# Kernel tuning notes

Measured on AMD Instinct MI355X. Metric: run time of the kernel, lower is better.

Reference implementation:

```python
import jax, jax.numpy as jnp
import numpy as np

B, H, CO, NV, NQ = 16, 1024, 512, 2048, 2048

def setup_inputs() -> dict:
    key = jax.random.key(0)
    ks = jax.random.split(key, 7)
    return {
        "V": jax.random.normal(ks[0], (B, H, NV), dtype=jnp.float32),
        "Q": jax.random.normal(ks[1], (B, NQ, H), dtype=jnp.float32),
        "W_b": jax.random.normal(ks[2], (H, H), dtype=jnp.float32),
        "W_v": jax.random.normal(ks[3], (CO, H), dtype=jnp.float32),
        "W_q": jax.random.normal(ks[4], (CO, H), dtype=jnp.float32),
        "w_hv": jax.random.normal(ks[5], (CO, 1), dtype=jnp.float32),
        "w_hq": jax.random.normal(ks[6], (CO, 1), dtype=jnp.float32),
    }

def reference(V, Q, W_b, W_v, W_q, w_hv, w_hq):
    # C = Q @ (W_b @ V): [B, Nq, Nv]
    WbV = jnp.einsum('hk,bkv->bhv', W_b, V)
    C = jnp.einsum('bqh,bhv->bqv', Q, WbV)
    WvV = jnp.einsum('ch,bhv->bcv', W_v, V)          # [B, CO, Nv]
    WqQt = jnp.einsum('ch,bqh->bcq', W_q, Q)         # [B, CO, Nq]
    H_v = jnp.tanh(WvV + jnp.einsum('bcq,bqv->bcv', WqQt, C))   # [B, CO, Nv]
    H_q = jnp.tanh(WqQt + jnp.einsum('bcv,bqv->bcq', WvV, C))   # [B, CO, Nq]
    a_v = jax.nn.softmax(jnp.einsum('c,bcv->bv', w_hv[:, 0], H_v), axis=-1)[:, None, :]  # [B,1,Nv]
    a_q = jax.nn.softmax(jnp.einsum('c,bcq->bq', w_hq[:, 0], H_q), axis=-1)[:, None, :]  # [B,1,Nq]
    v = jnp.einsum('bv,bhv->bh', a_v[:, 0], V)   # [B, H]
    q = jnp.einsum('bq,bqh->bh', a_q[:, 0], Q)   # [B, H]
    return (a_v, a_q, v, q)
```

## Files before the change

kernel.cpp:

```cpp
#include <hip/hip_runtime.h>
#include <math.h>

#define Bn  16
#define Hd  1024
#define COn 512
#define NVn 2048
#define NQn 2048

#define BM 128
#define BN 128
#define BK 16
#define LDT 132

typedef unsigned short u16;
typedef __attribute__((ext_vector_type(8))) short short8;
typedef __attribute__((ext_vector_type(4))) float floatx4;

__device__ __forceinline__ float fast_tanh(float x) {
    float ax = fabsf(x);
    float e  = __expf(2.0f * ax);
    float t  = 1.0f - 2.0f / (e + 1.0f);
    return copysignf(t, x);
}

__device__ __forceinline__ u16 f32_to_bf16(float x) {
    unsigned u = __float_as_uint(x);
    unsigned r = (u + 0x7fffu + ((u >> 16) & 1u)) >> 16;
    return (u16)r;
}
__device__ __forceinline__ float bf16_to_f32(u16 h) {
    return __uint_as_float(((unsigned)h) << 16);
}

__device__ __forceinline__ void gload16(const u16* g, u16* l) {
    __builtin_amdgcn_global_load_lds(
        (__attribute__((address_space(1))) void*)(g),
        (__attribute__((address_space(3))) void*)(l), 16, 0, 0);
}

template <bool LOGITS>
__global__ __launch_bounds__(512, 2) void mm8p(
    const u16* __restrict__ Ahp, const u16* __restrict__ Alp, long batchA, int ldA,
    const u16* __restrict__ Bhp, const u16* __restrict__ Blp, long batchB, int ldB,
    int N, int K, int gx, int gy,
    const float* __restrict__ bias,
    u16* __restrict__ Ch, u16* __restrict__ Cl, long batchC,
    const float* __restrict__ w, float* __restrict__ logits)
{
    __shared__ u16 lds[2][4][256 * 32];

    const int tid = threadIdx.x;
    const int nwg = (int)gridDim.x;
    int bid = (int)blockIdx.x;
    {
        int q = nwg >> 3, r = nwg & 7, xcd = bid & 7, idx = bid >> 3;
        bid = (xcd < r ? xcd * (q + 1) : r * (q + 1) + (xcd - r) * q) + idx;
    }
    const int bpz = gx * gy;
    const int b    = bid / bpz;
    const int brem = bid - b * bpz;
    const int m0 = (brem / gx) * 256;
    const int n0 = (brem % gx) * 256;

    const u16* Ahb = Ahp + (long)b * batchA;
    const u16* Alb = Alp + (long)b * batchA;
    const u16* Bhb = Bhp + (long)b * batchB;
    const u16* Blb = Blp + (long)b * batchB;

    const int wave = tid >> 6, lane = tid & 63;
    const int quad = lane >> 4, l16 = lane & 15;
    const int wm = (wave >> 2) * 128;
    const int wn = (wave & 3) * 64;
    const int aoff = quad * 8;

    const int smat  = wave >> 1;
    const int srow0 = (wave & 1) * 128;
    const int srl   = lane >> 2;
    const int ssl   = (lane & 3) * 8;
    const u16* srcp = smat == 0 ? Ahb : smat == 1 ? Alb : smat == 2 ? Bhb : Blb;
    const long sld  = (smat < 2) ? ldA : ldB;
    const int rowbase = (smat < 2) ? m0 : n0;
    const u16* sp = srcp + (long)(rowbase + srow0 + srl) * sld + ssl;

    floatx4 acc[8][4] = {};

#pragma unroll
    for (int j = 0; j < 8; ++j)
        gload16(sp + (long)j * 16 * sld, &lds[0][smat][(srow0 + j * 16) * 32]);
    asm volatile("s_waitcnt vmcnt(0)" ::: "memory");
    __builtin_amdgcn_s_barrier();

    const int NT = K >> 5;
    for (int t = 0; t < NT; ++t) {
        const int  cur = t & 1;
        const bool pf  = (t + 1 < NT);
        const long k0n = (long)(t + 1) * 32;
        const u16* Ah_ = &lds[cur][0][0];
        const u16* Al_ = &lds[cur][1][0];
        const u16* Bh_ = &lds[cur][2][0];
        const u16* Bl_ = &lds[cur][3][0];
        short8 bh[4], bl[4];
#pragma unroll
        for (int p = 0; p < 4; ++p) {
            if (p == 0) {
#pragma unroll
                for (int nt = 0; nt < 4; ++nt) {
                    const int br = (wn + nt * 16 + l16) * 32 + aoff;
                    bh[nt] = *(const short8*)&Bh_[br];
                    bl[nt] = *(const short8*)&Bl_[br];
                }
            }
            const int ar0 = (wm + (2 * p) * 16 + l16) * 32 + aoff;
            const int ar1 = ar0 + 16 * 32;
            const short8 a0h = *(const short8*)&Ah_[ar0];
            const short8 a0l = *(const short8*)&Al_[ar0];
            const short8 a1h = *(const short8*)&Ah_[ar1];
            const short8 a1l = *(const short8*)&Al_[ar1];
            if (pf && p < 2) {
                const int tb = cur ^ 1;
#pragma unroll
                for (int j = p * 4; j < p * 4 + 4; ++j)
                    gload16(sp + (long)j * 16 * sld + k0n,
                            &lds[tb][smat][(srow0 + j * 16) * 32]);
            }
            __builtin_amdgcn_s_barrier();
            __builtin_amdgcn_s_setprio(1);
#pragma unroll
            for (int nt = 0; nt < 4; ++nt) {
                floatx4 c0 = acc[2 * p][nt];
                c0 = __builtin_amdgcn_mfma_f32_16x16x32_bf16(a0h, bh[nt], c0, 0, 0, 0);
                c0 = __builtin_amdgcn_mfma_f32_16x16x32_bf16(a0h, bl[nt], c0, 0, 0, 0);
                c0 = __builtin_amdgcn_mfma_f32_16x16x32_bf16(a0l, bh[nt], c0, 0, 0, 0);
                acc[2 * p][nt] = c0;
                floatx4 c1 = acc[2 * p + 1][nt];
                c1 = __builtin_amdgcn_mfma_f32_16x16x32_bf16(a1h, bh[nt], c1, 0, 0, 0);
                c1 = __builtin_amdgcn_mfma_f32_16x16x32_bf16(a1h, bl[nt], c1, 0, 0, 0);
                c1 = __builtin_amdgcn_mfma_f32_16x16x32_bf16(a1l, bh[nt], c1, 0, 0, 0);
                acc[2 * p + 1][nt] = c1;
            }
            __builtin_amdgcn_s_setprio(0);
            if (p == 3 && pf) asm volatile("s_waitcnt vmcnt(0)" ::: "memory");
            __builtin_amdgcn_s_barrier();
        }
    }

    if constexpr (!LOGITS) {
        u16* Chb = Ch + (long)b * batchC;
        u16* Clb = Cl + (long)b * batchC;
#pragma unroll
        for (int mt = 0; mt < 8; ++mt)
#pragma unroll
            for (int nt = 0; nt < 4; ++nt)
#pragma unroll
                for (int r = 0; r < 4; ++r) {
                    const int row = m0 + wm + mt * 16 + quad * 4 + r;
                    const int col = n0 + wn + nt * 16 + l16;
                    float x = acc[mt][nt][r];
                    if (bias) x += bias[(long)row * N + col];
                    const u16 h = f32_to_bf16(x);
                    Chb[(long)row * N + col] = h;
                    Clb[(long)row * N + col] = f32_to_bf16(x - bf16_to_f32(h));
                }
    } else {
        float cs[4] = {};
#pragma unroll
        for (int nt = 0; nt < 4; ++nt)
#pragma unroll
            for (int mt = 0; mt < 8; ++mt)
#pragma unroll
                for (int r = 0; r < 4; ++r) {
                    const int row = m0 + wm + mt * 16 + quad * 4 + r;
                    cs[nt] = fmaf(w[row], fast_tanh(acc[mt][nt][r]), cs[nt]);
                }
        float* red = (float*)&lds[0][0][0];
        const int r8 = (wave >> 2) * 4 + quad;
#pragma unroll
        for (int nt = 0; nt < 4; ++nt)
            red[r8 * 256 + wn + nt * 16 + l16] = cs[nt];
        __syncthreads();
        if (tid < 256) {
            float s = 0.f;
#pragma unroll
            for (int r = 0; r < 8; ++r) s += red[r * 256 + tid];
            atomicAdd(logits + (long)b * N + n0 + tid, s);
        }
    }
}

template <bool LOGITS>
__global__ __launch_bounds__(256) void mm3(
    const u16* __restrict__ Ahp, const u16* __restrict__ Alp, long batchA, int ldA,
    const u16* __restrict__ Bhp, const u16* __restrict__ Blp, long batchB, int ldB,
    int N, int K,
    const float* __restrict__ bias,
    u16* __restrict__ Ch, u16* __restrict__ Cl, long batchC,
    const float* __restrict__ w, float* __restrict__ logits)
{
    __shared__ u16 Ah[128 * 32], Al[128 * 32], Bh[128 * 32], Bl[128 * 32];
    const int tid = threadIdx.x;
    const int b   = blockIdx.z;
    const int m0  = blockIdx.y * 128;
    const int n0  = blockIdx.x * 128;
    const u16* Ahb = Ahp + (long)b * batchA;
    const u16* Alb = Alp + (long)b * batchA;
    const u16* Bhb = Bhp + (long)b * batchB;
    const u16* Blb = Blp + (long)b * batchB;
    const int wave = tid >> 6, lane = tid & 63, quad = lane >> 4, l16 = lane & 15;
    const int wm = (wave >> 1) * 64, wn = (wave & 1) * 64;
    floatx4 acc[4][4] = {};

    for (int k0 = 0; k0 < K; k0 += 32) {
#pragma unroll
        for (int i = 0; i < 2; ++i) {
            int c = i * 256 + tid;
            int row = c >> 2, ko = (c & 3) * 8;
            long ga = (long)(m0 + row) * ldA + k0 + ko;
            long gb = (long)(n0 + row) * ldB + k0 + ko;
            *(short8*)&Ah[row * 32 + ko] = *(const short8*)&Ahb[ga];
            *(short8*)&Al[row * 32 + ko] = *(const short8*)&Alb[ga];
            *(short8*)&Bh[row * 32 + ko] = *(const short8*)&Bhb[gb];
            *(short8*)&Bl[row * 32 + ko] = *(const short8*)&Blb[gb];
        }
        __syncthreads();
        short8 ah[4], al[4], bh[4], bl[4];
#pragma unroll
        for (int t4 = 0; t4 < 4; ++t4) {
            int am = wm + t4 * 16 + l16;
            ah[t4] = *(const short8*)&Ah[am * 32 + quad * 8];
            al[t4] = *(const short8*)&Al[am * 32 + quad * 8];
            int bn = wn + t4 * 16 + l16;
            bh[t4] = *(const short8*)&Bh[bn * 32 + quad * 8];
            bl[t4] = *(const short8*)&Bl[bn * 32 + quad * 8];
        }
#pragma unroll
        for (int mt = 0; mt < 4; ++mt)
#pragma unroll
            for (int nt = 0; nt < 4; ++nt) {
                floatx4 a0 = acc[mt][nt];
                a0 = __builtin_amdgcn_mfma_f32_16x16x32_bf16(ah[mt], bh[nt], a0, 0, 0, 0);
                a0 = __builtin_amdgcn_mfma_f32_16x16x32_bf16(ah[mt], bl[nt], a0, 0, 0, 0);
                a0 = __builtin_amdgcn_mfma_f32_16x16x32_bf16(al[mt], bh[nt], a0, 0, 0, 0);
                acc[mt][nt] = a0;
            }
        __syncthreads();
    }

    if constexpr (!LOGITS) {
        u16* Chb = Ch + (long)b * batchC;
        u16* Clb = Cl + (long)b * batchC;
#pragma unroll
        for (int mt = 0; mt < 4; ++mt)
#pragma unroll
            for (int nt = 0; nt < 4; ++nt)
#pragma unroll
                for (int r = 0; r < 4; ++r) {
                    int row = m0 + wm + mt * 16 + quad * 4 + r;
                    int col = n0 + wn + nt * 16 + l16;
                    float x = acc[mt][nt][r];
                    if (bias) x += bias[(long)row * N + col];
                    u16 h = f32_to_bf16(x);
                    u16 l = f32_to_bf16(x - bf16_to_f32(h));
                    Chb[(long)row * N + col] = h;
                    Clb[(long)row * N + col] = l;
                }
    } else {
        float cs[4] = {};
#pragma unroll
        for (int nt = 0; nt < 4; ++nt)
#pragma unroll
            for (int mt = 0; mt < 4; ++mt)
#pragma unroll
                for (int r = 0; r < 4; ++r) {
                    int row = m0 + wm + mt * 16 + quad * 4 + r;
                    cs[nt] = fmaf(w[row], fast_tanh(acc[mt][nt][r]), cs[nt]);
                }
        float* red = (float*)Ah;
        const int r8 = (wave >> 1) * 4 + quad;
#pragma unroll
        for (int nt = 0; nt < 4; ++nt)
            red[r8 * 128 + wn + nt * 16 + l16] = cs[nt];
        __syncthreads();
        if (tid < 128) {
            float s = 0.f;
#pragma unroll
            for (int r = 0; r < 8; ++r) s += red[r * 128 + tid];
            atomicAdd(logits + (long)b * N + n0 + tid, s);
        }
    }
}

__global__ __launch_bounds__(256) void split_kernel(
    const float* __restrict__ X, u16* __restrict__ Xh, u16* __restrict__ Xl)
{
    long i0 = ((long)blockIdx.x * 256 + threadIdx.x) * 4;
    float4 v = *(const float4*)(X + i0);
    float xs[4] = {v.x, v.y, v.z, v.w};
    u16 h[4], l[4];
#pragma unroll
    for (int i = 0; i < 4; ++i) {
        h[i] = f32_to_bf16(xs[i]);
        l[i] = f32_to_bf16(xs[i] - bf16_to_f32(h[i]));
    }
    *(ushort4*)(Xh + i0) = *(ushort4*)h;
    *(ushort4*)(Xl + i0) = *(ushort4*)l;
}

__global__ __launch_bounds__(256) void tsplit_kernel(
    const float* __restrict__ src, u16* __restrict__ dh, u16* __restrict__ dl,
    int R, int C)
{
    __shared__ float tile[64][65];
    const int b = blockIdx.z;
    const int r0 = blockIdx.x * 64, c0 = blockIdx.y * 64;
    const float* S = src + (long)b * R * C;
    const int t = threadIdx.x;
    const int lr = t >> 2, lc0 = (t & 3) * 16;
#pragma unroll
    for (int i = 0; i < 4; ++i)
        *(float4*)&tile[lr][lc0 + i * 4] =
            *(const float4*)(S + (long)(r0 + lr) * C + c0 + lc0 + i * 4);
    __syncthreads();
    u16 hbuf[16], lbuf[16];
#pragma unroll
    for (int i = 0; i < 16; ++i) {
        float x = tile[lc0 + i][lr];
        u16 hi = f32_to_bf16(x);
        hbuf[i] = hi;
        lbuf[i] = f32_to_bf16(x - bf16_to_f32(hi));
    }
    long o = (long)b * R * C + (long)(c0 + lr) * R + r0 + lc0;
    *(short8*)(dh + o)     = *(short8*)&hbuf[0];
    *(short8*)(dh + o + 8) = *(short8*)&hbuf[8];
    *(short8*)(dl + o)     = *(short8*)&lbuf[0];
    *(short8*)(dl + o + 8) = *(short8*)&lbuf[8];
}

template <bool LOGITS>
__global__ __launch_bounds__(256) void gemm_core(
    const float* __restrict__ A, const float* __restrict__ Bm, float* __restrict__ C,
    const float* __restrict__ bias,
    int M, int N, int K,
    int sAm, int sAk, long batchA,
    int sBk, int sBn, long batchB,
    long batchC,
    const float* __restrict__ w, float* __restrict__ logits)
{
    __shared__ float As[BK][LDT];
    __shared__ float Bs[BK][LDT];
    const int tid = threadIdx.x;
    const int b   = blockIdx.z;
    const int m0  = blockIdx.y * BM;
    const int n0  = blockIdx.x * BN;
    const float* Ab = A  + (long)b * batchA;
    const float* Bb = Bm + (long)b * batchB;
    const int tm = tid >> 4, tn = tid & 15;
    float acc[8][8] = {};

    for (int k0 = 0; k0 < K; k0 += BK) {
        if (sAk == 1) {
#pragma unroll
            for (int i = 0; i < 2; ++i) {
                int idx = tid + i * 256;
                int m = idx >> 2, kg = (idx & 3) * 4;
                float4 v = *(const float4*)(Ab + (long)(m0 + m) * sAm + k0 + kg);
                As[kg+0][m] = v.x; As[kg+1][m] = v.y; As[kg+2][m] = v.z; As[kg+3][m] = v.w;
            }
        } else {
#pragma unroll
            for (int i = 0; i < 2; ++i) {
                int idx = tid + i * 256;
                int k = idx >> 5, mg = (idx & 31) * 4;
                float4 v = *(const float4*)(Ab + (long)(k0 + k) * sAk + m0 + mg);
                *(float4*)&As[k][mg] = v;
            }
        }
        if (sBn == 1) {
#pragma unroll
            for (int i = 0; i < 2; ++i) {
                int idx = tid + i * 256;
                int k = idx >> 5, ng = (idx & 31) * 4;
                float4 v = *(const float4*)(Bb + (long)(k0 + k) * sBk + n0 + ng);
                *(float4*)&Bs[k][ng] = v;
            }
        } else {
#pragma unroll
            for (int i = 0; i < 2; ++i) {
                int idx = tid + i * 256;
                int n = idx >> 2, kg = (idx & 3) * 4;
                float4 v = *(const float4*)(Bb + (long)(n0 + n) * sBn + k0 + kg);
                Bs[kg+0][n] = v.x; Bs[kg+1][n] = v.y; Bs[kg+2][n] = v.z; Bs[kg+3][n] = v.w;
            }
        }
        __syncthreads();
#pragma unroll
        for (int kk = 0; kk < BK; ++kk) {
            float a[8], bv[8];
            *(float4*)&a[0]  = *(const float4*)&As[kk][tm * 4];
            *(float4*)&a[4]  = *(const float4*)&As[kk][64 + tm * 4];
            *(float4*)&bv[0] = *(const float4*)&Bs[kk][tn * 4];
            *(float4*)&bv[4] = *(const float4*)&Bs[kk][64 + tn * 4];
#pragma unroll
            for (int i = 0; i < 8; ++i)
#pragma unroll
                for (int j = 0; j < 8; ++j)
                    acc[i][j] = fmaf(a[i], bv[j], acc[i][j]);
        }
        __syncthreads();
    }

    if constexpr (!LOGITS) {
        float* Cb = C + (long)b * batchC;
#pragma unroll
        for (int i = 0; i < 8; ++i) {
            int row = m0 + (i >> 2) * 64 + tm * 4 + (i & 3);
            float* crow = Cb + (long)row * N + n0;
            float4 o0 = {acc[i][0], acc[i][1], acc[i][2], acc[i][3]};
            float4 o1 = {acc[i][4], acc[i][5], acc[i][6], acc[i][7]};
            if (bias) {
                const float* brow = bias + (long)row * N + n0;
                float4 b0 = *(const float4*)(brow + tn * 4);
                float4 b1 = *(const float4*)(brow + 64 + tn * 4);
                o0.x += b0.x; o0.y += b0.y; o0.z += b0.z; o0.w += b0.w;
                o1.x += b1.x; o1.y += b1.y; o1.z += b1.z; o1.w += b1.w;
            }
            *(float4*)(crow + tn * 4) = o0;
            *(float4*)(crow + 64 + tn * 4) = o1;
        }
    } else {
        float wv[8];
#pragma unroll
        for (int i = 0; i < 8; ++i) wv[i] = w[m0 + (i >> 2) * 64 + tm * 4 + (i & 3)];
        float cs[8];
#pragma unroll
        for (int j = 0; j < 8; ++j) {
            float s = 0.f;
#pragma unroll
            for (int i = 0; i < 8; ++i) s = fmaf(wv[i], fast_tanh(acc[i][j]), s);
            cs[j] = s;
        }
        __syncthreads();
        *(float4*)&As[tm][tn * 4]      = *(float4*)&cs[0];
        *(float4*)&As[tm][64 + tn * 4] = *(float4*)&cs[4];
        __syncthreads();
        if (tid < 128) {
            float s = 0.f;
#pragma unroll
            for (int r = 0; r < 16; ++r) s += As[r][tid];
            atomicAdd(logits + (long)b * N + n0 + tid, s);
        }
    }
}

__global__ __launch_bounds__(256) void softmax_kernel(
    const float* __restrict__ lv, const float* __restrict__ lq, float* __restrict__ out)
{
    const int b = blockIdx.x;
    const int which = blockIdx.y;
    const float* x = (which == 0 ? lv : lq) + (long)b * 2048;
    float* o = out + (long)which * (Bn * 2048) + (long)b * 2048;
    const int tid = threadIdx.x;
    __shared__ float sm[4], ss[4];

    float m = -3.4e38f;
    for (int i = tid; i < 2048; i += 256) m = fmaxf(m, x[i]);
    for (int off = 32; off > 0; off >>= 1) m = fmaxf(m, __shfl_down(m, off));
    if ((tid & 63) == 0) sm[tid >> 6] = m;
    __syncthreads();
    m = fmaxf(fmaxf(sm[0], sm[1]), fmaxf(sm[2], sm[3]));

    float s = 0.f;
    for (int i = tid; i < 2048; i += 256) s += expf(x[i] - m);
    for (int off = 32; off > 0; off >>= 1) s += __shfl_down(s, off);
    if ((tid & 63) == 0) ss[tid >> 6] = s;
    __syncthreads();
    s = ss[0] + ss[1] + ss[2] + ss[3];
    float inv = 1.0f / s;
    for (int i = tid; i < 2048; i += 256) o[i] = expf(x[i] - m) * inv;
}

__global__ __launch_bounds__(256) void vout_kernel(
    const float* __restrict__ V, const float* __restrict__ av, float* __restrict__ vout)
{
    const int wave = threadIdx.x >> 6, lane = threadIdx.x & 63;
    const long idx = (long)blockIdx.x * 4 + wave;
    const int b = (int)(idx >> 10);
    const int h = (int)(idx & 1023);
    const float* vp = V + ((long)b * Hd + h) * NVn;
    const float* ap = av + (long)b * NVn;
    float s = 0.f;
    for (int i = lane; i < NVn; i += 64) s = fmaf(ap[i], vp[i], s);
    for (int off = 32; off > 0; off >>= 1) s += __shfl_down(s, off);
    if (lane == 0) vout[idx] = s;
}

__global__ __launch_bounds__(256) void qout_kernel(
    const float* __restrict__ Q, const float* __restrict__ aq, float* __restrict__ qout)
{
    const int h  = blockIdx.x * 256 + threadIdx.x;
    const int b  = blockIdx.z;
    const int q0 = blockIdx.y * 256;
    const float* qp = Q + (long)b * NQn * Hd;
    const float* ap = aq + (long)b * NQn + q0;
    float s = 0.f;
    for (int q = 0; q < 256; ++q) s = fmaf(ap[q], qp[(long)(q0 + q) * Hd + h], s);
    atomicAdd(qout + (long)b * Hd + h, s);
}

extern "C" void kernel_launch(void* const* d_in, const int* in_sizes, int n_in,
                              void* d_out, int out_size, void* d_ws, size_t ws_size,
                              hipStream_t stream) {
    const float* V    = (const float*)d_in[0];
    const float* Q    = (const float*)d_in[1];
    const float* W_b  = (const float*)d_in[2];
    const float* W_v  = (const float*)d_in[3];
    const float* W_q  = (const float*)d_in[4];
    const float* w_hv = (const float*)d_in[5];
    const float* w_hq = (const float*)d_in[6];
    float* out = (float*)d_out;
    dim3 blk(256);

    const long BIG  = (long)Bn * Hd * NVn;
    const long GEL  = (long)Bn * Hd * Hd;
    const long TEL  = (long)Bn * COn * Hd;
    const long WQE  = (long)COn * Hd;
    const long WBE  = (long)Hd * Hd;

    u16* ws16 = (u16*)d_ws;
    u16* R1h  = ws16;            u16* R1l  = R1h + BIG;
    u16* Gh   = R1l + BIG;       u16* Gl   = Gh + GEL;
    u16* Th   = Gl + GEL;        u16* Tl   = Th + TEL;
    u16* Uh   = Gh;              u16* Ul   = Gh + TEL;
    u16* Wqh  = Tl + TEL;        u16* Wql  = Wqh + WQE;
    u16* Wvh  = Wql + WQE;       u16* Wvl  = Wvh + WQE;
    u16* Wbh  = Wvl + WQE;       u16* Wbl  = Wbh + WBE;
    u16* WbTh = Wbl + WBE;       u16* WbTl = WbTh + WBE;
    float* lv = (float*)(WbTl + WBE);
    float* lq = lv + Bn * NVn;
    const size_t need = (size_t)((u16*)(lq + Bn * NQn) - ws16) * 2;

    float* vout_p = out + 2 * Bn * NVn;
    float* qout_p = vout_p + Bn * Hd;

    if (ws_size >= need) {
        hipMemsetAsync(lv, 0, (size_t)(Bn * NVn + Bn * NQn) * sizeof(float), stream);
        hipMemsetAsync(qout_p, 0, (size_t)Bn * Hd * sizeof(float), stream);

        split_kernel<<<dim3((unsigned)(WQE / 1024)), blk, 0, stream>>>(W_q, Wqh, Wql);
        split_kernel<<<dim3((unsigned)(WQE / 1024)), blk, 0, stream>>>(W_v, Wvh, Wvl);
        split_kernel<<<dim3((unsigned)(WBE / 1024)), blk, 0, stream>>>(W_b, Wbh, Wbl);
        tsplit_kernel<<<dim3(Hd / 64, Hd / 64, 1), blk, 0, stream>>>(W_b, WbTh, WbTl, Hd, Hd);

        tsplit_kernel<<<dim3(NQn / 64, Hd / 64, Bn), blk, 0, stream>>>(Q, R1h, R1l, NQn, Hd);
        mm8p<false><<<dim3((Hd / 256) * (Hd / 256) * Bn), dim3(512), 0, stream>>>(
            R1h, R1l, (long)Hd * NQn, NQn,  R1h, R1l, (long)Hd * NQn, NQn,
            Hd, NQn, Hd / 256, Hd / 256,
            nullptr, Gh, Gl, (long)Hd * Hd, nullptr, nullptr);
        mm3<false><<<dim3(Hd / 128, COn / 128, Bn), blk, 0, stream>>>(
            Wqh, Wql, 0L, Hd,  Gh, Gl, (long)Hd * Hd, Hd,
            Hd, Hd, nullptr, Th, Tl, (long)COn * Hd, nullptr, nullptr);
        mm3<false><<<dim3(Hd / 128, COn / 128, Bn), blk, 0, stream>>>(
            Th, Tl, (long)COn * Hd, Hd,  WbTh, WbTl, 0L, Hd,
            Hd, Hd, W_v, Uh, Ul, (long)COn * Hd, nullptr, nullptr);
        tsplit_kernel<<<dim3(Hd / 64, NVn / 64, Bn), blk, 0, stream>>>(V, R1h, R1l, Hd, NVn);
        mm8p<true><<<dim3((NVn / 256) * (COn / 256) * Bn), dim3(512), 0, stream>>>(
            Uh, Ul, (long)COn * Hd, Hd,  R1h, R1l, (long)NVn * Hd, Hd,
            NVn, Hd, NVn / 256, COn / 256,
            nullptr, nullptr, nullptr, 0L, w_hv, lv);

        split_kernel<<<dim3((unsigned)(BIG / 1024)), blk, 0, stream>>>(V, R1h, R1l);
        mm8p<false><<<dim3((Hd / 256) * (Hd / 256) * Bn), dim3(512), 0, stream>>>(
            R1h, R1l, (long)Hd * NVn, NVn,  R1h, R1l, (long)Hd * NVn, NVn,
            Hd, NVn, Hd / 256, Hd / 256,
            nullptr, Gh, Gl, (long)Hd * Hd, nullptr, nullptr);
        mm3<false><<<dim3(Hd / 128, COn / 128, Bn), blk, 0, stream>>>(
            Wvh, Wvl, 0L, Hd,  Gh, Gl, (long)Hd * Hd, Hd,
            Hd, Hd, nullptr, Th, Tl, (long)COn * Hd, nullptr, nullptr);
        mm3<false><<<dim3(Hd / 128, COn / 128, Bn), blk, 0, stream>>>(
            Th, Tl, (long)COn * Hd, Hd,  Wbh, Wbl, 0L, Hd,
            Hd, Hd, W_q, Uh, Ul, (long)COn * Hd, nullptr, nullptr);
        split_kernel<<<dim3((unsigned)(BIG / 1024)), blk, 0, stream>>>(Q, R1h, R1l);
        mm8p<true><<<dim3((NQn / 256) * (COn / 256) * Bn), dim3(512), 0, stream>>>(
            Uh, Ul, (long)COn * Hd, Hd,  R1h, R1l, (long)NQn * Hd, Hd,
            NQn, Hd, NQn / 256, COn / 256,
            nullptr, nullptr, nullptr, 0L, w_hq, lq);

        softmax_kernel<<<dim3(Bn, 2), blk, 0, stream>>>(lv, lq, out);
        vout_kernel<<<dim3(Bn * Hd / 4), blk, 0, stream>>>(V, out, vout_p);
        qout_kernel<<<dim3(Hd / 256, NQn / 256, Bn), blk, 0, stream>>>(Q, out + Bn * NVn, qout_p);
        return;
    }

    float* ws = (float*)d_ws;
    float* g  = ws;
    float* t  = g + GEL;
    float* u  = t + TEL;
    float* flv = u + TEL;
    float* flq = flv + Bn * NVn;

    hipMemsetAsync(flv, 0, (size_t)(Bn * NVn + Bn * NQn) * sizeof(float), stream);
    hipMemsetAsync(qout_p, 0, (size_t)Bn * Hd * sizeof(float), stream);

    gemm_core<false><<<dim3(Hd/BN, Hd/BM, Bn), blk, 0, stream>>>(Q, Q, g, nullptr,
        Hd, Hd, NQn, 1, Hd, (long)NQn*Hd, Hd, 1, (long)NQn*Hd, (long)Hd*Hd, nullptr, nullptr);
    gemm_core<false><<<dim3(Hd/BN, COn/BM, Bn), blk, 0, stream>>>(W_q, g, t, nullptr,
        COn, Hd, Hd, Hd, 1, 0L, Hd, 1, (long)Hd*Hd, (long)COn*Hd, nullptr, nullptr);
    gemm_core<false><<<dim3(Hd/BN, COn/BM, Bn), blk, 0, stream>>>(t, W_b, u, W_v,
        COn, Hd, Hd, Hd, 1, (long)COn*Hd, Hd, 1, 0L, (long)COn*Hd, nullptr, nullptr);
    gemm_core<true><<<dim3(NVn/BN, COn/BM, Bn), blk, 0, stream>>>(
        u, V, nullptr, nullptr, COn, NVn, Hd,
        Hd, 1, (long)COn*Hd, NVn, 1, (long)Hd*NVn, 0L, w_hv, flv);
    gemm_core<false><<<dim3(Hd/BN, Hd/BM, Bn), blk, 0, stream>>>(V, V, g, nullptr,
        Hd, Hd, NVn, NVn, 1, (long)Hd*NVn, 1, NVn, (long)Hd*NVn, (long)Hd*Hd, nullptr, nullptr);
    gemm_core<false><<<dim3(Hd/BN, COn/BM, Bn), blk, 0, stream>>>(W_v, g, t, nullptr,
        COn, Hd, Hd, Hd, 1, 0L, Hd, 1, (long)Hd*Hd, (long)COn*Hd, nullptr, nullptr);
    gemm_core<false><<<dim3(Hd/BN, COn/BM, Bn), blk, 0, stream>>>(t, W_b, u, W_q,
        COn, Hd, Hd, Hd, 1, (long)COn*Hd, 1, Hd, 0L, (long)COn*Hd, nullptr, nullptr);
    gemm_core<true><<<dim3(NQn/BN, COn/BM, Bn), blk, 0, stream>>>(
        u, Q, nullptr, nullptr, COn, NQn, Hd,
        Hd, 1, (long)COn*Hd, 1, Hd, (long)NQn*Hd, 0L, w_hq, flq);

    softmax_kernel<<<dim3(Bn, 2), blk, 0, stream>>>(flv, flq, out);
    vout_kernel<<<dim3(Bn * Hd / 4), blk, 0, stream>>>(V, out, vout_p);
    qout_kernel<<<dim3(Hd / 256, NQn / 256, Bn), blk, 0, stream>>>(Q, out + Bn * NVn, qout_p);
}
```

Measured before the change: 1.275 ms.

## XOR-swizzle LDS tiles and issue full prefetch once per K-step

Applies an XOR swizzle to the K-chunk position of both the staged LDS tiles and the fragment reads, in both GEMM kernels, so that lanes reading 16-byte fragments hit different LDS banks. The swizzle is applied on the global-read side for the direct-to-LDS loads. The main kernel also issues all eight prefetch loads at once after loading B fragments, and drops the per-phase barriers, leaving a single wait and barrier per K-step. The aim is fewer bank conflicts and less synchronisation, at the risk of less even interleaving of memory traffic with MFMA work.

```diff
diff --git a/kernel.cpp b/kernel.cpp
--- a/kernel.cpp
+++ b/kernel.cpp
@@ -69,18 +69,18 @@
 
     const int wave = tid >> 6, lane = tid & 63;
     const int quad = lane >> 4, l16 = lane & 15;
+    const int xsl = (quad ^ ((l16 >> 1) & 3)) * 8;
     const int wm = (wave >> 2) * 128;
     const int wn = (wave & 3) * 64;
-    const int aoff = quad * 8;
 
     const int smat  = wave >> 1;
     const int srow0 = (wave & 1) * 128;
     const int srl   = lane >> 2;
-    const int ssl   = (lane & 3) * 8;
+    const int kx    = ((lane & 3) ^ ((lane >> 3) & 3)) * 8;
     const u16* srcp = smat == 0 ? Ahb : smat == 1 ? Alb : smat == 2 ? Bhb : Blb;
     const long sld  = (smat < 2) ? ldA : ldB;
     const int rowbase = (smat < 2) ? m0 : n0;
-    const u16* sp = srcp + (long)(rowbase + srow0 + srl) * sld + ssl;
+    const u16* sp = srcp + (long)(rowbase + srow0 + srl) * sld + kx;
 
     floatx4 acc[8][4] = {};
 
@@ -99,31 +99,28 @@
         const u16* Al_ = &lds[cur][1][0];
         const u16* Bh_ = &lds[cur][2][0];
         const u16* Bl_ = &lds[cur][3][0];
+
         short8 bh[4], bl[4];
 #pragma unroll
+        for (int nt = 0; nt < 4; ++nt) {
+            const int bs = (wn + nt * 16 + l16) * 32 + xsl;
+            bh[nt] = *(const short8*)&Bh_[bs];
+            bl[nt] = *(const short8*)&Bl_[bs];
+        }
+        if (pf) {
+            u16* dst = &lds[cur ^ 1][smat][srow0 * 32];
+#pragma unroll
+            for (int j = 0; j < 8; ++j)
+                gload16(sp + (long)j * 16 * sld + k0n, dst + j * 16 * 32);
+        }
+#pragma unroll
         for (int p = 0; p < 4; ++p) {
-            if (p == 0) {
-#pragma unroll
-                for (int nt = 0; nt < 4; ++nt) {
-                    const int br = (wn + nt * 16 + l16) * 32 + aoff;
-                    bh[nt] = *(const short8*)&Bh_[br];
-                    bl[nt] = *(const short8*)&Bl_[br];
-                }
-            }
-            const int ar0 = (wm + (2 * p) * 16 + l16) * 32 + aoff;
-            const int ar1 = ar0 + 16 * 32;
-            const short8 a0h = *(const short8*)&Ah_[ar0];
-            const short8 a0l = *(const short8*)&Al_[ar0];
-            const short8 a1h = *(const short8*)&Ah_[ar1];
-            const short8 a1l = *(const short8*)&Al_[ar1];
-            if (pf && p < 2) {
-                const int tb = cur ^ 1;
-#pragma unroll
-                for (int j = p * 4; j < p * 4 + 4; ++j)
-                    gload16(sp + (long)j * 16 * sld + k0n,
-                            &lds[tb][smat][(srow0 + j * 16) * 32]);
-            }
-            __builtin_amdgcn_s_barrier();
+            const int as0 = (wm + p * 32 + l16) * 32 + xsl;
+            const int as1 = as0 + 16 * 32;
+            const short8 a0h = *(const short8*)&Ah_[as0];
+            const short8 a0l = *(const short8*)&Al_[as0];
+            const short8 a1h = *(const short8*)&Ah_[as1];
+            const short8 a1l = *(const short8*)&Al_[as1];
             __builtin_amdgcn_s_setprio(1);
 #pragma unroll
             for (int nt = 0; nt < 4; ++nt) {
@@ -139,9 +136,9 @@
                 acc[2 * p + 1][nt] = c1;
             }
             __builtin_amdgcn_s_setprio(0);
-            if (p == 3 && pf) asm volatile("s_waitcnt vmcnt(0)" ::: "memory");
-            __builtin_amdgcn_s_barrier();
-        }
+        }
+        if (pf) asm volatile("s_waitcnt vmcnt(0)" ::: "memory");
+        __builtin_amdgcn_s_barrier();
     }
 
     if constexpr (!LOGITS) {
@@ -206,6 +203,7 @@
     const u16* Bhb = Bhp + (long)b * batchB;
     const u16* Blb = Blp + (long)b * batchB;
     const int wave = tid >> 6, lane = tid & 63, quad = lane >> 4, l16 = lane & 15;
+    const int xsl = (quad ^ ((l16 >> 1) & 3)) * 8;
     const int wm = (wave >> 1) * 64, wn = (wave & 1) * 64;
     floatx4 acc[4][4] = {};
 
@@ -213,24 +211,25 @@
 #pragma unroll
         for (int i = 0; i < 2; ++i) {
             int c = i * 256 + tid;
-            int row = c >> 2, ko = (c & 3) * 8;
-            long ga = (long)(m0 + row) * ldA + k0 + ko;
-            long gb = (long)(n0 + row) * ldB + k0 + ko;
-            *(short8*)&Ah[row * 32 + ko] = *(const short8*)&Ahb[ga];
-            *(short8*)&Al[row * 32 + ko] = *(const short8*)&Alb[ga];
-            *(short8*)&Bh[row * 32 + ko] = *(const short8*)&Bhb[gb];
-            *(short8*)&Bl[row * 32 + ko] = *(const short8*)&Blb[gb];
+            int row = c >> 2, u = c & 3;
+            int g = u ^ ((row >> 1) & 3);
+            long ga = (long)(m0 + row) * ldA + k0 + g * 8;
+            long gb = (long)(n0 + row) * ldB + k0 + g * 8;
+            *(short8*)&Ah[row * 32 + u * 8] = *(const short8*)&Ahb[ga];
+            *(short8*)&Al[row * 32 + u * 8] = *(const short8*)&Alb[ga];
+            *(short8*)&Bh[row * 32 + u * 8] = *(const short8*)&Bhb[gb];
+            *(short8*)&Bl[row * 32 + u * 8] = *(const short8*)&Blb[gb];
         }
         __syncthreads();
         short8 ah[4], al[4], bh[4], bl[4];
 #pragma unroll
         for (int t4 = 0; t4 < 4; ++t4) {
-            int am = wm + t4 * 16 + l16;
-            ah[t4] = *(const short8*)&Ah[am * 32 + quad * 8];
-            al[t4] = *(const short8*)&Al[am * 32 + quad * 8];
-            int bn = wn + t4 * 16 + l16;
-            bh[t4] = *(const short8*)&Bh[bn * 32 + quad * 8];
-            bl[t4] = *(const short8*)&Bl[bn * 32 + quad * 8];
+            const int as = (wm + t4 * 16 + l16) * 32 + xsl;
+            ah[t4] = *(const short8*)&Ah[as];
+            al[t4] = *(const short8*)&Al[as];
+            const int bs = (wn + t4 * 16 + l16) * 32 + xsl;
+            bh[t4] = *(const short8*)&Bh[bs];
+            bl[t4] = *(const short8*)&Bl[bs];
         }
 #pragma unroll
         for (int mt = 0; mt < 4; ++mt)
```

Result: no change. 1.257 ms (-1.4%).
